# Optimization experiments

Hardware: AMD Instinct MI355X
Metric: run time of the kernel (lower is better)

The kernel has to match this reference:

```python
import jax, jax.numpy as jnp
import numpy as np

B, C, H, W = 4, 512, 96, 96
NH = 8
HD = C // NH
NC = 128
D = 768
L = H * W
EPS = 1e-5  # torch LayerNorm default


def _l2n(x, axis):
    # F.normalize: x / max(||x||, 1e-12)
    return x / jnp.maximum(jnp.linalg.norm(x, axis=axis, keepdims=True), 1e-12)


def _ln2d(x, g, b):
    # LayerNorm2d: normalize over channel dim of (B,C,H,W)
    mu = x.mean(1, keepdims=True)
    var = ((x - mu) ** 2).mean(1, keepdims=True)
    return (x - mu) / jnp.sqrt(var + EPS) * g[None, :, None, None] + b[None, :, None, None]


def _conv1x1(x, w):
    return jnp.einsum('oc,bchw->bohw', w, x)


def setup_inputs() -> dict:
    key = jax.random.key(0)
    ks = jax.random.split(key, 9)
    s = 0.02
    return {
        'img_feats': jax.random.normal(ks[0], (B, C, H, W), jnp.float32),
        'cls_embs': jax.random.normal(ks[1], (NC, D), jnp.float32),
        'cls_logits': jax.random.normal(ks[2], (B, NC), jnp.float32),
        'seg_logits': jax.random.normal(ks[3], (B, 1, H, W), jnp.float32),
        'gamma_g': jnp.ones((D,), jnp.float32), 'beta_g': jnp.zeros((D,), jnp.float32),
        'gamma_f': jnp.ones((C,), jnp.float32), 'beta_f': jnp.zeros((C,), jnp.float32),
        'attn_scale': jnp.ones((NH, 1, 1), jnp.float32),
        'Wg': jax.random.normal(ks[4], (C, D), jnp.float32) * s,
        'Wqkv': jax.random.normal(ks[5], (3 * C, C), jnp.float32) * s,
        'Wo': jax.random.normal(ks[6], (C, C), jnp.float32) * s,
        'bo': jnp.zeros((C,), jnp.float32),
        'gamma_n': jnp.ones((C,), jnp.float32), 'beta_n': jnp.zeros((C,), jnp.float32),
        'W1': jax.random.normal(ks[7], (C, C), jnp.float32) * s, 'b1': jnp.zeros((C,), jnp.float32),
        'W2': jax.random.normal(ks[8], (C, C), jnp.float32) * s, 'b2': jnp.zeros((C,), jnp.float32),
    }


def reference(img_feats, cls_embs, cls_logits, seg_logits, gamma_g, beta_g,
              gamma_f, beta_f, attn_scale, Wg, Wqkv, Wo, bo, gamma_n, beta_n,
              W1, b1, W2, b2):
    xn = _ln2d(img_feats, gamma_f, beta_f)
    # guide LayerNorm over embedding dim
    mu = cls_embs.mean(-1, keepdims=True)
    var = ((cls_embs - mu) ** 2).mean(-1, keepdims=True)
    cn = (cls_embs - mu) / jnp.sqrt(var + EPS) * gamma_g + beta_g
    g = (cn @ Wg.T).reshape(NC, NH, HD)  # nc nh hd

    qkv = _conv1x1(xn, Wqkv).reshape(B, 3, NH, HD, L)
    q, k, v = qkv[:, 0], qkv[:, 1], qkv[:, 2]  # each (B,NH,HD,L)

    # cosine guide map + min-max normalization + softmax-weighted aggregation over classes
    gm = jnp.einsum('nhd,bhdl->bhnl', _l2n(g, -1), _l2n(q, -2))
    gm = gm - gm.min(-1, keepdims=True)
    gm = gm / gm.max(-1, keepdims=True)
    gm = (jax.nn.softmax(gm, axis=2) * gm).sum(2, keepdims=True)  # (B,NH,1,L)

    # auxiliary guide map from cls logits + masked pooling of k
    cls_obj = jnp.einsum('nhd,bn->bhd', g, cls_logits)
    mask = jax.nn.sigmoid(seg_logits)  # (B,1,H,W)
    seg_obj = (mask * k.reshape(B, C, H, W)).sum((2, 3)) / mask.sum((2, 3))  # (B,C)
    obj = _l2n(cls_obj + seg_obj.reshape(B, NH, HD), -1)
    aux = jnp.einsum('bhd,bhdl->bhl', obj, _l2n(k, -2))[:, :, None, :]
    aux = aux - aux.min(-1, keepdims=True)
    aux = aux / aux.max(-1, keepdims=True)
    gm = gm * aux

    v = gm * v
    # channel (transposed) cosine attention: (B,NH,HD,HD)
    attn = jnp.einsum('bhdl,bhel->bhde', _l2n(q, -1), _l2n(k, -1)) * attn_scale
    out = jnp.einsum('bhde,bhel->bhdl', jax.nn.softmax(attn, -1), v).reshape(B, C, H, W)

    x = img_feats + _conv1x1(out, Wo) + bo[None, :, None, None]
    # ConvMlp with pre-norm: LayerNorm2d -> 1x1 conv -> GELU -> 1x1 conv
    fin = _ln2d(x, gamma_n, beta_n)
    h = jax.nn.gelu(_conv1x1(fin, W1) + b1[None, :, None, None], approximate=False)
    return x + _conv1x1(h, W2) + b2[None, :, None, None]
```

## Files before the change

kernel.cpp:

```cpp
#include <hip/hip_runtime.h>
#include <hip/hip_bf16.h>
#include <math.h>

#define BB 4
#define CC 512
#define NHEAD 8
#define HDIM 64
#define NCLS 128
#define DD 768
#define LL 9216
#define BLPIX 36864
#define EPSV 1e-5f
#define GMBLK 144
#define AUXBLK 36
#define LSPLIT 8

typedef __hip_bfloat16 bf16;
typedef __attribute__((ext_vector_type(8))) short short8v;
typedef __attribute__((ext_vector_type(4))) short short4v;
typedef __attribute__((ext_vector_type(4))) float f32x4;

__device__ __forceinline__ float bf2f(bf16 v){ return __bfloat162float(v); }
__device__ __forceinline__ bf16 f2bf(float v){ return __float2bfloat16(v); }
__device__ __forceinline__ short bfbits(float v){ bf16 b = __float2bfloat16(v); return *reinterpret_cast<short*>(&b); }
__device__ __forceinline__ float s2f(short s){ bf16 b = *reinterpret_cast<bf16*>(&s); return __bfloat162float(b); }

__global__ void ln_stats_k(const float* __restrict__ X, float* __restrict__ mu, float* __restrict__ rs){
  int idx = blockIdx.x * blockDim.x + threadIdx.x;
  if (idx >= BLPIX) return;
  int b = idx / LL, l = idx % LL;
  const float* p = X + (size_t)b * CC * LL + l;
  float s = 0.f, ss = 0.f;
  #pragma unroll 8
  for (int c = 0; c < CC; c++){ float v = p[(size_t)c * LL]; s += v; ss += v * v; }
  float m = s * (1.0f / CC);
  float var = ss * (1.0f / CC) - m * m;
  mu[idx] = m; rs[idx] = rsqrtf(var + EPSV);
}

__global__ __launch_bounds__(256) void lnT_k(const float* __restrict__ X,
    const float* __restrict__ mu, const float* __restrict__ rs,
    const float* __restrict__ lng, const float* __restrict__ lnb,
    bf16* __restrict__ out){
  __shared__ float t[64][65];
  int c0 = blockIdx.x * 64;
  int p0 = blockIdx.y * 64;
  int b = p0 / LL;
  int l0 = p0 - b * LL;
  int tid = threadIdx.x;
  #pragma unroll
  for (int i = 0; i < 16; i++){
    int idx = i * 256 + tid;
    int cl = idx >> 6, ll2 = idx & 63;
    t[cl][ll2] = X[(size_t)b * CC * LL + (size_t)(c0 + cl) * LL + l0 + ll2];
  }
  __syncthreads();
  int pr = tid >> 4;
  int cc = (tid & 15) * 4;
  #pragma unroll
  for (int i = 0; i < 4; i++){
    int pl = pr + i * 16;
    int p = p0 + pl;
    float m = mu[p], r = rs[p];
    short4v pk;
    #pragma unroll
    for (int e = 0; e < 4; e++){
      int c = c0 + cc + e;
      float v = (t[cc + e][pl] - m) * r * lng[c] + lnb[c];
      pk[e] = bfbits(v);
    }
    *(short4v*)&out[(size_t)p * CC + c0 + cc] = pk;
  }
}

__global__ void wcast_k(const float* __restrict__ wqkv, const float* __restrict__ wo,
                        const float* __restrict__ w1, const float* __restrict__ w2,
                        bf16* __restrict__ oq, bf16* __restrict__ oo,
                        bf16* __restrict__ o1, bf16* __restrict__ o2){
  int i = blockIdx.x * 256 + threadIdx.x;
  int e = i * 4;
  const float* src; bf16* dst; int off;
  if (e < 786432){ src = wqkv; dst = oq; off = e; }
  else if (e < 1048576){ src = wo; dst = oo; off = e - 786432; }
  else if (e < 1310720){ src = w1; dst = o1; off = e - 1048576; }
  else { src = w2; dst = o2; off = e - 1310720; }
  float4 v = *reinterpret_cast<const float4*>(src + off);
  short4v pk;
  pk[0] = bfbits(v.x); pk[1] = bfbits(v.y); pk[2] = bfbits(v.z); pk[3] = bfbits(v.w);
  *(short4v*)&dst[off] = pk;
}

__global__ void statsred_k(const float2* __restrict__ statp, float* __restrict__ mu, float* __restrict__ rs){
  int p = blockIdx.x * 256 + threadIdx.x;
  if (p >= BLPIX) return;
  float s = 0.f, ss = 0.f;
  #pragma unroll
  for (int part = 0; part < 4; part++){
    float2 v = statp[part * BLPIX + p];
    s += v.x; ss += v.y;
  }
  float m = s * (1.0f / CC);
  float var = ss * (1.0f / CC) - m * m;
  mu[p] = m; rs[p] = rsqrtf(var + EPSV);
}

template<int MODE>
__global__ __launch_bounds__(256, 2) void mgemm_k(
    const bf16* __restrict__ A,
    const bf16* __restrict__ B,
    const float* __restrict__ residf,
    const bf16*  __restrict__ residb,
    const float* __restrict__ bias,
    const float* __restrict__ mu, const float* __restrict__ rs,
    const float* __restrict__ lng, const float* __restrict__ lnb,
    float2* __restrict__ statp,
    bf16* __restrict__ qo, bf16* __restrict__ ko, bf16* __restrict__ vo,
    bf16* __restrict__ xT_out,
    float* __restrict__ xo,
    bf16* __restrict__ ho)
{
  __shared__ short Asm[128 * 64];
  __shared__ short Bsm[128 * 64];
  __shared__ float sred[4][4][16][2];
  int tid = threadIdx.x;
  int lane = tid & 63, wv = tid >> 6;
  int wr = wv >> 1, wc = wv & 1;
  int r15 = lane & 15, g = lane >> 4, h7 = lane & 7;
  int gx = gridDim.x;
  int flat = blockIdx.y * gx + blockIdx.x;
  int cpx = (gx * gridDim.y) >> 3;
  int swz = (flat & 7) * cpx + (flat >> 3);
  int m0 = (swz % gx) * 128, n0 = (swz / gx) * 128;
  int srow = tid >> 3, skkg = tid & 7;
  int sslot = ((skkg ^ (srow & 7))) * 8;

  f32x4 acc[4][4];
  #pragma unroll
  for (int i = 0; i < 4; i++)
    #pragma unroll
    for (int j = 0; j < 4; j++) acc[i][j] = (f32x4){0.f, 0.f, 0.f, 0.f};

  short8v pa[4], pb[4];
  auto loadAB = [&](int it){
    int k0 = it * 64;
    if (MODE == 2){
      int c0 = k0 + skkg * 8;
      float ga[8], be[8];
      *(float4*)&ga[0] = *(const float4*)&lng[c0];
      *(float4*)&ga[4] = *(const float4*)&lng[c0 + 4];
      *(float4*)&be[0] = *(const float4*)&lnb[c0];
      *(float4*)&be[4] = *(const float4*)&lnb[c0 + 4];
      #pragma unroll
      for (int r = 0; r < 4; r++){
        pa[r] = *reinterpret_cast<const short8v*>(A + (size_t)(m0 + r * 32 + srow) * 512 + c0);
        int rp = n0 + r * 32 + srow;
        float mm = mu[rp], rr = rs[rp];
        short8v raw = *reinterpret_cast<const short8v*>(B + (size_t)rp * 512 + c0);
        short8v ov;
        #pragma unroll
        for (int e = 0; e < 8; e++){
          float v = (s2f(raw[e]) - mm) * rr * ga[e] + be[e];
          ov[e] = bfbits(v);
        }
        pb[r] = ov;
      }
    } else {
      #pragma unroll
      for (int r = 0; r < 4; r++){
        pa[r] = *reinterpret_cast<const short8v*>(A + (size_t)(m0 + r * 32 + srow) * 512 + k0 + skkg * 8);
        pb[r] = *reinterpret_cast<const short8v*>(B + (size_t)(n0 + r * 32 + srow) * 512 + k0 + skkg * 8);
      }
    }
  };

  loadAB(0);
  for (int it = 0; it < 8; ++it){
    __syncthreads();
    #pragma unroll
    for (int r = 0; r < 4; r++){
      int row = r * 32 + srow;
      *(short8v*)&Asm[row * 64 + sslot] = pa[r];
      *(short8v*)&Bsm[row * 64 + sslot] = pb[r];
    }
    __syncthreads();
    if (it < 7) loadAB(it + 1);
    #pragma unroll
    for (int s = 0; s < 2; s++){
      int slot = ((s * 4 + g) ^ h7) * 8;
      short8v af[4], bf_[4];
      #pragma unroll
      for (int i = 0; i < 4; i++){
        af[i]  = *(const short8v*)&Asm[(wr * 64 + i * 16 + r15) * 64 + slot];
        bf_[i] = *(const short8v*)&Bsm[(wc * 64 + i * 16 + r15) * 64 + slot];
      }
      #pragma unroll
      for (int i = 0; i < 4; i++)
        #pragma unroll
        for (int j = 0; j < 4; j++){
          if (MODE == 2)
            acc[i][j] = __builtin_amdgcn_mfma_f32_16x16x32_bf16(bf_[i], af[j], acc[i][j], 0, 0, 0);
          else
            acc[i][j] = __builtin_amdgcn_mfma_f32_16x16x32_bf16(af[i], bf_[j], acc[i][j], 0, 0, 0);
        }
    }
  }

  int bIdx = n0 / LL;
  int lbase = n0 - bIdx * LL;
  if (MODE == 0){
    int part = m0 >> 9;
    if (part < 2){
      bf16* dst = (part == 0) ? qo : ko;
      int chb = (m0 & 511) + wr * 64;
      #pragma unroll
      for (int i = 0; i < 4; i++)
        #pragma unroll
        for (int j = 0; j < 4; j++){
          int l = lbase + wc * 64 + j * 16 + r15;
          #pragma unroll
          for (int e = 0; e < 4; e++){
            int ch = chb + i * 16 + g * 4 + e;
            dst[(size_t)bIdx * CC * LL + (size_t)ch * LL + l] = f2bf(acc[i][j][e]);
          }
        }
    } else {
      int chb = (m0 & 511) + wr * 64;
      #pragma unroll
      for (int i = 0; i < 4; i++)
        #pragma unroll
        for (int j = 0; j < 4; j++){
          int l = lbase + wc * 64 + j * 16 + r15;
          int ch = chb + i * 16 + g * 4;
          short4v pk;
          #pragma unroll
          for (int e = 0; e < 4; e++) pk[e] = bfbits(acc[i][j][e]);
          *(short4v*)&vo[((size_t)bIdx * LL + l) * CC + ch] = pk;
        }
    }
  } else if (MODE == 1){
    float sj[4] = {0.f,0.f,0.f,0.f}, ssj[4] = {0.f,0.f,0.f,0.f};
    #pragma unroll
    for (int i = 0; i < 4; i++)
      #pragma unroll
      for (int j = 0; j < 4; j++){
        int l = lbase + wc * 64 + j * 16 + r15;
        int chm = m0 + wr * 64 + i * 16 + g * 4;
        short4v pk;
        #pragma unroll
        for (int e = 0; e < 4; e++){
          int m = chm + e;
          size_t o = (size_t)bIdx * CC * LL + (size_t)m * LL + l;
          float xv = residf[o] + acc[i][j][e] + bias[m];
          pk[e] = bfbits(xv);
          sj[j] += xv; ssj[j] += xv * xv;
        }
        *(short4v*)&xT_out[((size_t)bIdx * LL + l) * CC + chm] = pk;
      }
    #pragma unroll
    for (int j = 0; j < 4; j++){
      sj[j] += __shfl_xor(sj[j], 16); sj[j] += __shfl_xor(sj[j], 32);
      ssj[j] += __shfl_xor(ssj[j], 16); ssj[j] += __shfl_xor(ssj[j], 32);
    }
    if (g == 0){
      #pragma unroll
      for (int j = 0; j < 4; j++){ sred[wv][j][r15][0] = sj[j]; sred[wv][j][r15][1] = ssj[j]; }
    }
    __syncthreads();
    if (tid < 128){
      int wv2 = tid >> 6, lane2 = tid & 63, j2 = lane2 >> 4, r2 = lane2 & 15;
      float s = sred[wv2][j2][r2][0] + sred[wv2 + 2][j2][r2][0];
      float ss2 = sred[wv2][j2][r2][1] + sred[wv2 + 2][j2][r2][1];
      int p = n0 + wv2 * 64 + j2 * 16 + r2;
      statp[(m0 >> 7) * BLPIX + p] = make_float2(s, ss2);
    }
  } else if (MODE == 3){
    #pragma unroll
    for (int i = 0; i < 4; i++)
      #pragma unroll
      for (int j = 0; j < 4; j++){
        int l = lbase + wc * 64 + j * 16 + r15;
        int chm = m0 + wr * 64 + i * 16 + g * 4;
        short4v rv = *(const short4v*)&residb[((size_t)bIdx * LL + l) * CC + chm];
        #pragma unroll
        for (int e = 0; e < 4; e++){
          int m = chm + e;
          size_t o = (size_t)bIdx * CC * LL + (size_t)m * LL + l;
          xo[o] = s2f(rv[e]) + acc[i][j][e] + bias[m];
        }
      }
  } else {
    #pragma unroll
    for (int i = 0; i < 4; i++)
      #pragma unroll
      for (int j = 0; j < 4; j++){
        int mm = m0 + wr * 64 + j * 16 + r15;
        float bv = bias[mm];
        #pragma unroll
        for (int e = 0; e < 4; e++){
          int n = n0 + wc * 64 + i * 16 + g * 4 + e;
          float t = acc[i][j][e] + bv;
          float gv = 0.5f * t * (1.0f + erff(t * 0.70710678118654752f));
          ho[(size_t)n * CC + mm] = f2bf(gv);
        }
      }
  }
}

__global__ void rownorm_k(const bf16* __restrict__ q, const bf16* __restrict__ k,
                          float* __restrict__ qn, float* __restrict__ kn){
  __shared__ float red[256];
  int row = blockIdx.x;
  const bf16* src = (row < 2048) ? q : k;
  int r = (row < 2048) ? row : row - 2048;
  const bf16* p = src + (size_t)r * LL;
  float s = 0.f;
  for (int i = threadIdx.x; i < LL; i += 256){ float v = bf2f(p[i]); s += v * v; }
  red[threadIdx.x] = s; __syncthreads();
  for (int st = 128; st > 0; st >>= 1){ if (threadIdx.x < st) red[threadIdx.x] += red[threadIdx.x + st]; __syncthreads(); }
  if (threadIdx.x == 0){
    float nv = fmaxf(sqrtf(red[0]), 1e-12f);
    if (row < 2048) qn[r] = nv; else kn[r] = nv;
  }
}

__global__ void clsg_k(const float* __restrict__ cls_embs, const float* __restrict__ gamma_g,
                       const float* __restrict__ beta_g, const float* __restrict__ Wg,
                       float* __restrict__ g, bf16* __restrict__ gnb){
  __shared__ float cn[DD];
  __shared__ float red[256];
  __shared__ float gsh[CC];
  __shared__ float nrm[NHEAD];
  int n = blockIdx.x;
  const float* e = cls_embs + (size_t)n * DD;
  float s = 0.f, ss = 0.f;
  for (int i = threadIdx.x; i < DD; i += 256){ float v = e[i]; s += v; ss += v * v; }
  red[threadIdx.x] = s; __syncthreads();
  for (int st = 128; st > 0; st >>= 1){ if (threadIdx.x < st) red[threadIdx.x] += red[threadIdx.x + st]; __syncthreads(); }
  float mean = red[0] / DD; __syncthreads();
  red[threadIdx.x] = ss; __syncthreads();
  for (int st = 128; st > 0; st >>= 1){ if (threadIdx.x < st) red[threadIdx.x] += red[threadIdx.x + st]; __syncthreads(); }
  float var = red[0] / DD - mean * mean;
  float rstd = rsqrtf(var + EPSV);
  __syncthreads();
  for (int i = threadIdx.x; i < DD; i += 256) cn[i] = (e[i] - mean) * rstd * gamma_g[i] + beta_g[i];
  __syncthreads();
  for (int c = threadIdx.x; c < CC; c += 256){
    const float* w = Wg + (size_t)c * DD;
    float a = 0.f;
    #pragma unroll 8
    for (int d = 0; d < DD; d++) a += cn[d] * w[d];
    gsh[c] = a;
  }
  __syncthreads();
  if (threadIdx.x < NHEAD){
    float a = 0.f;
    for (int d = 0; d < HDIM; d++){ float v = gsh[threadIdx.x * HDIM + d]; a += v * v; }
    nrm[threadIdx.x] = fmaxf(sqrtf(a), 1e-12f);
  }
  __syncthreads();
  for (int c = threadIdx.x; c < CC; c += 256){
    g[(size_t)n * CC + c] = gsh[c];
    gnb[(size_t)n * CC + c] = f2bf(gsh[c] / nrm[c >> 6]);
  }
}

__global__ void clsobj_k(const float* __restrict__ g, const float* __restrict__ cls_l,
                         float* __restrict__ cls_obj){
  int idx = blockIdx.x * 256 + threadIdx.x;
  if (idx >= BB * CC) return;
  int b = idx >> 9, c = idx & 511;
  float a = 0.f;
  for (int n = 0; n < NCLS; n++) a += g[(size_t)n * CC + c] * cls_l[b * NCLS + n];
  cls_obj[idx] = a;
}

__global__ __launch_bounds__(256) void gm1_k(const bf16* __restrict__ q, const bf16* __restrict__ gnb,
        float* __restrict__ pmin, float* __restrict__ pmax){
  __shared__ bf16 qs[64 * 68];
  __shared__ float sspart[4][64];
  __shared__ float rq[64];
  int bh = blockIdx.x, lt = blockIdx.y;
  int l0 = lt * 64;
  int t = threadIdx.x;
  int b = bh >> 3, h = bh & 7;
  int w = t >> 6, lane = t & 63, r15 = lane & 15, g = lane >> 4;
  const bf16* qp = q + (size_t)b * CC * LL + (size_t)h * HDIM * LL + l0;
  #pragma unroll
  for (int i2 = 0; i2 < 4; i2++){
    int idx = t + i2 * 256;
    int d = idx >> 4, lch = (idx & 15) * 4;
    short4v vv = *reinterpret_cast<const short4v*>(qp + (size_t)d * LL + lch);
    *(short4v*)&qs[d * 68 + lch] = vv;
  }
  __syncthreads();
  {
    int l = t & 63, dg = t >> 6;
    float ss = 0.f;
    #pragma unroll
    for (int dd = 0; dd < 16; dd++){ float v = bf2f(qs[(dg * 16 + dd) * 68 + l]); ss += v * v; }
    sspart[dg][l] = ss;
  }
  __syncthreads();
  if (t < 64){
    float ss = sspart[0][t] + sspart[1][t] + sspart[2][t] + sspart[3][t];
    rq[t] = 1.0f / fmaxf(sqrtf(ss), 1e-12f);
  }
  __syncthreads();
  short8v ag[2][2];
  #pragma unroll
  for (int i = 0; i < 2; i++)
    #pragma unroll
    for (int kt = 0; kt < 2; kt++)
      ag[i][kt] = *reinterpret_cast<const short8v*>(gnb + (size_t)(w * 32 + i * 16 + r15) * CC + h * 64 + kt * 32 + g * 8);
  short8v bq[4][2];
  #pragma unroll
  for (int j = 0; j < 4; j++){
    float rqv = rq[j * 16 + r15];
    #pragma unroll
    for (int kt = 0; kt < 2; kt++){
      short8v bb;
      #pragma unroll
      for (int jj = 0; jj < 8; jj++){
        int d = kt * 32 + g * 8 + jj;
        bb[jj] = bfbits(bf2f(qs[d * 68 + j * 16 + r15]) * rqv);
      }
      bq[j][kt] = bb;
    }
  }
  f32x4 acc[2][4];
  #pragma unroll
  for (int i = 0; i < 2; i++)
    #pragma unroll
    for (int j = 0; j < 4; j++) acc[i][j] = (f32x4){0.f,0.f,0.f,0.f};
  #pragma unroll
  for (int kt = 0; kt < 2; kt++)
    #pragma unroll
    for (int i = 0; i < 2; i++)
      #pragma unroll
      for (int j = 0; j < 4; j++)
        acc[i][j] = __builtin_amdgcn_mfma_f32_16x16x32_bf16(ag[i][kt], bq[j][kt], acc[i][j], 0, 0, 0);
  #pragma unroll
  for (int i = 0; i < 2; i++)
    #pragma unroll
    for (int e = 0; e < 4; e++){
      float mn = acc[i][0][e], mx = acc[i][0][e];
      #pragma unroll
      for (int j = 1; j < 4; j++){ mn = fminf(mn, acc[i][j][e]); mx = fmaxf(mx, acc[i][j][e]); }
      #pragma unroll
      for (int msk = 1; msk < 16; msk <<= 1){
        mn = fminf(mn, __shfl_xor(mn, msk));
        mx = fmaxf(mx, __shfl_xor(mx, msk));
      }
      if (r15 == 0){
        int n = w * 32 + i * 16 + g * 4 + e;
        pmin[((size_t)bh * 128 + n) * GMBLK + lt] = mn;
        pmax[((size_t)bh * 128 + n) * GMBLK + lt] = mx;
      }
    }
}

__global__ void gmred_k(const float* __restrict__ pmin, const float* __restrict__ pmax,
                        float* __restrict__ gmin, float* __restrict__ gms){
  __shared__ float rmn[64], rmx[64];
  int row = blockIdx.x;
  float mn = 1e30f, mx = -1e30f;
  for (int i = threadIdx.x; i < GMBLK; i += 64){
    mn = fminf(mn, pmin[(size_t)row * GMBLK + i]);
    mx = fmaxf(mx, pmax[(size_t)row * GMBLK + i]);
  }
  rmn[threadIdx.x] = mn; rmx[threadIdx.x] = mx; __syncthreads();
  for (int st = 32; st > 0; st >>= 1){
    if (threadIdx.x < st){
      rmn[threadIdx.x] = fminf(rmn[threadIdx.x], rmn[threadIdx.x + st]);
      rmx[threadIdx.x] = fmaxf(rmx[threadIdx.x], rmx[threadIdx.x + st]);
    }
    __syncthreads();
  }
  if (threadIdx.x == 0){ gmin[row] = rmn[0]; gms[row] = rmx[0] - rmn[0]; }
}

__global__ void seg_k(const float* __restrict__ seg, const bf16* __restrict__ k, float* __restrict__ seg_num){
  __shared__ float red[256];
  int bc = blockIdx.x;
  int b = bc >> 9;
  const bf16* p = k + (size_t)bc * LL;
  const float* sp = seg + (size_t)b * LL;
  float s = 0.f;
  for (int i = threadIdx.x; i < LL; i += 256){
    float m = 1.0f / (1.0f + expf(-sp[i]));
    s += m * bf2f(p[i]);
  }
  red[threadIdx.x] = s; __syncthreads();
  for (int st = 128; st > 0; st >>= 1){ if (threadIdx.x < st) red[threadIdx.x] += red[threadIdx.x + st]; __syncthreads(); }
  if (threadIdx.x == 0) seg_num[bc] = red[0];
}

__global__ void segden_k(const float* __restrict__ seg, float* __restrict__ den){
  __shared__ float red[256];
  int b = blockIdx.x;
  const float* sp = seg + (size_t)b * LL;
  float s = 0.f;
  for (int i = threadIdx.x; i < LL; i += 256) s += 1.0f / (1.0f + expf(-sp[i]));
  red[threadIdx.x] = s; __syncthreads();
  for (int st = 128; st > 0; st >>= 1){ if (threadIdx.x < st) red[threadIdx.x] += red[threadIdx.x + st]; __syncthreads(); }
  if (threadIdx.x == 0) den[b] = red[0];
}

__global__ void obj_k(const float* __restrict__ cls_obj, const float* __restrict__ seg_num,
                      const float* __restrict__ den, float* __restrict__ obj){
  __shared__ float sval[2048];
  __shared__ float nrm[32];
  int tid = threadIdx.x;
  #pragma unroll
  for (int i = 0; i < 8; i++){
    int idx = tid + i * 256;
    int b = idx >> 9;
    sval[idx] = cls_obj[idx] + seg_num[idx] / den[b];
  }
  __syncthreads();
  if (tid < 32){
    float s = 0.f;
    for (int d = 0; d < 64; d++){ float v = sval[tid * 64 + d]; s += v * v; }
    nrm[tid] = fmaxf(sqrtf(s), 1e-12f);
  }
  __syncthreads();
  #pragma unroll
  for (int i = 0; i < 8; i++){
    int idx = tid + i * 256;
    obj[idx] = sval[idx] / nrm[idx >> 6];
  }
}

__global__ void aux_k(const bf16* __restrict__ k, const float* __restrict__ obj, float* __restrict__ aux,
                      float* __restrict__ pmin, float* __restrict__ pmax){
  __shared__ float os[64];
  __shared__ float rmn[256], rmx[256];
  int bh = blockIdx.x, lt = blockIdx.y;
  int b = bh >> 3, h = bh & 7;
  int l = lt * 256 + threadIdx.x;
  if (threadIdx.x < 64) os[threadIdx.x] = obj[bh * 64 + threadIdx.x];
  __syncthreads();
  const bf16* kp = k + (size_t)b * CC * LL + (size_t)h * HDIM * LL + l;
  float ss = 0.f, dot = 0.f;
  #pragma unroll 8
  for (int d = 0; d < 64; d++){ float v = bf2f(kp[(size_t)d * LL]); ss += v * v; dot += os[d] * v; }
  float av = dot / fmaxf(sqrtf(ss), 1e-12f);
  aux[(size_t)bh * LL + l] = av;
  rmn[threadIdx.x] = av; rmx[threadIdx.x] = av; __syncthreads();
  for (int st = 128; st > 0; st >>= 1){
    if (threadIdx.x < st){
      rmn[threadIdx.x] = fminf(rmn[threadIdx.x], rmn[threadIdx.x + st]);
      rmx[threadIdx.x] = fmaxf(rmx[threadIdx.x], rmx[threadIdx.x + st]);
    }
    __syncthreads();
  }
  if (threadIdx.x == 0){ pmin[bh * AUXBLK + lt] = rmn[0]; pmax[bh * AUXBLK + lt] = rmx[0]; }
}

__global__ void auxred_k(const float* __restrict__ pmin, const float* __restrict__ pmax,
                         float* __restrict__ amin, float* __restrict__ ams){
  __shared__ float rmn[64], rmx[64];
  int bh = blockIdx.x;
  float mn = 1e30f, mx = -1e30f;
  for (int i = threadIdx.x; i < AUXBLK; i += 64){
    mn = fminf(mn, pmin[bh * AUXBLK + i]);
    mx = fmaxf(mx, pmax[bh * AUXBLK + i]);
  }
  rmn[threadIdx.x] = mn; rmx[threadIdx.x] = mx; __syncthreads();
  for (int st = 32; st > 0; st >>= 1){
    if (threadIdx.x < st){
      rmn[threadIdx.x] = fminf(rmn[threadIdx.x], rmn[threadIdx.x + st]);
      rmx[threadIdx.x] = fmaxf(rmx[threadIdx.x], rmx[threadIdx.x + st]);
    }
    __syncthreads();
  }
  if (threadIdx.x == 0){ amin[bh] = rmn[0]; ams[bh] = rmx[0] - rmn[0]; }
}

__global__ __launch_bounds__(256) void attn_k(const bf16* __restrict__ q, const bf16* __restrict__ k,
                                              float* __restrict__ part){
  __shared__ float red[4 * 4096];
  int ls = blockIdx.x, bh = blockIdx.y;
  int b = bh >> 3, h = bh & 7;
  int t = threadIdx.x;
  int w = t >> 6, lane = t & 63, r15 = lane & 15, g = lane >> 4;
  const bf16* qp = q + (size_t)b * CC * LL + (size_t)h * HDIM * LL;
  const bf16* kp = k + (size_t)b * CC * LL + (size_t)h * HDIM * LL;
  int kbase = ls * 1152 + w * 288;
  f32x4 acc[4][4];
  #pragma unroll
  for (int i = 0; i < 4; i++)
    #pragma unroll
    for (int j = 0; j < 4; j++) acc[i][j] = (f32x4){0.f,0.f,0.f,0.f};
  for (int ks = 0; ks < 9; ks++){
    int koff = kbase + ks * 32 + g * 8;
    short8v aq[4], bk[4];
    #pragma unroll
    for (int i = 0; i < 4; i++) aq[i] = *reinterpret_cast<const short8v*>(qp + (size_t)(i * 16 + r15) * LL + koff);
    #pragma unroll
    for (int j = 0; j < 4; j++) bk[j] = *reinterpret_cast<const short8v*>(kp + (size_t)(j * 16 + r15) * LL + koff);
    #pragma unroll
    for (int i = 0; i < 4; i++)
      #pragma unroll
      for (int j = 0; j < 4; j++)
        acc[i][j] = __builtin_amdgcn_mfma_f32_16x16x32_bf16(aq[i], bk[j], acc[i][j], 0, 0, 0);
  }
  #pragma unroll
  for (int i = 0; i < 4; i++)
    #pragma unroll
    for (int j = 0; j < 4; j++)
      #pragma unroll
      for (int e = 0; e < 4; e++)
        red[w * 4096 + (i * 16 + g * 4 + e) * 64 + j * 16 + r15] = acc[i][j][e];
  __syncthreads();
  #pragma unroll
  for (int it = 0; it < 16; it++){
    int idx = t + it * 256;
    part[((size_t)(bh * LSPLIT + ls)) * 4096 + idx] = red[idx] + red[4096 + idx] + red[8192 + idx] + red[12288 + idx];
  }
}

__global__ void smax_k(const float* __restrict__ part, const float* __restrict__ qn,
                       const float* __restrict__ kn, const float* __restrict__ scale,
                       bf16* __restrict__ Pb){
  __shared__ float As[64 * 65];
  int bh = blockIdx.x;
  int h = bh & 7;
  int tid = threadIdx.x;
  #pragma unroll
  for (int i = 0; i < 16; i++){
    int cell = tid + i * 256;
    int d = cell >> 6, e = cell & 63;
    float s = 0.f;
    #pragma unroll
    for (int ls = 0; ls < LSPLIT; ls++) s += part[((size_t)(bh * LSPLIT + ls)) * 4096 + cell];
    As[d * 65 + e] = s * scale[h] / (qn[bh * 64 + d] * kn[bh * 64 + e]);
  }
  __syncthreads();
  if (tid < 64){
    int d = tid;
    float mx = -1e30f;
    for (int e = 0; e < 64; e++) mx = fmaxf(mx, As[d * 65 + e]);
    float sum = 0.f;
    for (int e = 0; e < 64; e++){ float ev = expf(As[d * 65 + e] - mx); As[d * 65 + e] = ev; sum += ev; }
    float inv = 1.0f / sum;
    for (int e = 0; e < 64; e++) Pb[(size_t)bh * 4096 + d * 64 + e] = f2bf(As[d * 65 + e] * inv);
  }
}

__global__ __launch_bounds__(256) void pv_k(const bf16* __restrict__ q, const bf16* __restrict__ gnb,
      const float* __restrict__ aux,
      const float* __restrict__ gmin, const float* __restrict__ gms,
      const float* __restrict__ amin, const float* __restrict__ ams,
      const bf16* __restrict__ Pb, const bf16* __restrict__ vT, bf16* __restrict__ outT){
  __shared__ bf16 qs[64 * 68];
  __shared__ float sspart[4][64];
  __shared__ float rq[64];
  __shared__ float gminS[128], rgmsS[128];
  __shared__ float separt[4][64], setpart[4][64];
  __shared__ float wl[64];
  int bh = blockIdx.x, lt = blockIdx.y;
  int l0 = lt * 64;
  int t = threadIdx.x;
  int b = bh >> 3, h = bh & 7;
  int w = t >> 6, lane = t & 63, r15 = lane & 15, g = lane >> 4;
  if (t < 128){ gminS[t] = gmin[bh * 128 + t]; rgmsS[t] = 1.0f / gms[bh * 128 + t]; }
  const bf16* qp = q + (size_t)b * CC * LL + (size_t)h * HDIM * LL + l0;
  #pragma unroll
  for (int i2 = 0; i2 < 4; i2++){
    int idx = t + i2 * 256;
    int d = idx >> 4, lch = (idx & 15) * 4;
    short4v vv = *reinterpret_cast<const short4v*>(qp + (size_t)d * LL + lch);
    *(short4v*)&qs[d * 68 + lch] = vv;
  }
  __syncthreads();
  {
    int l = t & 63, dg = t >> 6;
    float ss = 0.f;
    #pragma unroll
    for (int dd = 0; dd < 16; dd++){ float v = bf2f(qs[(dg * 16 + dd) * 68 + l]); ss += v * v; }
    sspart[dg][l] = ss;
  }
  __syncthreads();
  if (t < 64){
    float ss = sspart[0][t] + sspart[1][t] + sspart[2][t] + sspart[3][t];
    rq[t] = 1.0f / fmaxf(sqrtf(ss), 1e-12f);
  }
  __syncthreads();
  short8v ag[2][2];
  #pragma unroll
  for (int i = 0; i < 2; i++)
    #pragma unroll
    for (int kt = 0; kt < 2; kt++)
      ag[i][kt] = *reinterpret_cast<const short8v*>(gnb + (size_t)(w * 32 + i * 16 + r15) * CC + h * 64 + kt * 32 + g * 8);
  short8v bq[4][2];
  #pragma unroll
  for (int j = 0; j < 4; j++){
    float rqv = rq[j * 16 + r15];
    #pragma unroll
    for (int kt = 0; kt < 2; kt++){
      short8v bb;
      #pragma unroll
      for (int jj = 0; jj < 8; jj++){
        int d = kt * 32 + g * 8 + jj;
        bb[jj] = bfbits(bf2f(qs[d * 68 + j * 16 + r15]) * rqv);
      }
      bq[j][kt] = bb;
    }
  }
  f32x4 acc[2][4];
  #pragma unroll
  for (int i = 0; i < 2; i++)
    #pragma unroll
    for (int j = 0; j < 4; j++) acc[i][j] = (f32x4){0.f,0.f,0.f,0.f};
  #pragma unroll
  for (int kt = 0; kt < 2; kt++)
    #pragma unroll
    for (int i = 0; i < 2; i++)
      #pragma unroll
      for (int j = 0; j < 4; j++)
        acc[i][j] = __builtin_amdgcn_mfma_f32_16x16x32_bf16(ag[i][kt], bq[j][kt], acc[i][j], 0, 0, 0);
  float seL[4] = {0.f,0.f,0.f,0.f}, setL[4] = {0.f,0.f,0.f,0.f};
  #pragma unroll
  for (int i = 0; i < 2; i++)
    #pragma unroll
    for (int j = 0; j < 4; j++)
      #pragma unroll
      for (int e = 0; e < 4; e++){
        int n = w * 32 + i * 16 + g * 4 + e;
        float tt = (acc[i][j][e] - gminS[n]) * rgmsS[n];
        float ee = __expf(tt);
        seL[j] += ee; setL[j] += ee * tt;
      }
  #pragma unroll
  for (int j = 0; j < 4; j++){
    seL[j] += __shfl_xor(seL[j], 16); seL[j] += __shfl_xor(seL[j], 32);
    setL[j] += __shfl_xor(setL[j], 16); setL[j] += __shfl_xor(setL[j], 32);
  }
  if (g == 0){
    #pragma unroll
    for (int j = 0; j < 4; j++){ separt[w][j * 16 + r15] = seL[j]; setpart[w][j * 16 + r15] = setL[j]; }
  }
  __syncthreads();
  if (t < 64){
    float se = separt[0][t] + separt[1][t] + separt[2][t] + separt[3][t];
    float st = setpart[0][t] + setpart[1][t] + setpart[2][t] + setpart[3][t];
    float gmred = st / se;
    float auxn = (aux[(size_t)bh * LL + l0 + t] - amin[bh]) / ams[bh];
    wl[t] = gmred * auxn;
  }
  __syncthreads();
  short8v ap[4][2];
  #pragma unroll
  for (int i = 0; i < 4; i++)
    #pragma unroll
    for (int kt = 0; kt < 2; kt++)
      ap[i][kt] = *reinterpret_cast<const short8v*>(Pb + (size_t)bh * 4096 + (i * 16 + r15) * 64 + kt * 32 + g * 8);
  const bf16* vrow = vT + ((size_t)b * LL + l0 + w * 16 + r15) * CC + h * 64;
  short8v bv[2];
  #pragma unroll
  for (int kt = 0; kt < 2; kt++) bv[kt] = *reinterpret_cast<const short8v*>(vrow + kt * 32 + g * 8);
  f32x4 oacc[4];
  #pragma unroll
  for (int i = 0; i < 4; i++) oacc[i] = (f32x4){0.f,0.f,0.f,0.f};
  #pragma unroll
  for (int kt = 0; kt < 2; kt++)
    #pragma unroll
    for (int i = 0; i < 4; i++)
      oacc[i] = __builtin_amdgcn_mfma_f32_16x16x32_bf16(ap[i][kt], bv[kt], oacc[i], 0, 0, 0);
  float wlv = wl[w * 16 + r15];
  bf16* orow = outT + ((size_t)b * LL + l0 + w * 16 + r15) * CC + h * 64;
  #pragma unroll
  for (int i = 0; i < 4; i++){
    short4v pk;
    #pragma unroll
    for (int e = 0; e < 4; e++) pk[e] = bfbits(oacc[i][e] * wlv);
    *(short4v*)&orow[i * 16 + g * 4] = pk;
  }
}

extern "C" void kernel_launch(void* const* d_in, const int* in_sizes, int n_in,
                              void* d_out, int out_size, void* d_ws, size_t ws_size,
                              hipStream_t stream){
  const float* img        = (const float*)d_in[0];
  const float* cls_embs   = (const float*)d_in[1];
  const float* cls_logits = (const float*)d_in[2];
  const float* seg        = (const float*)d_in[3];
  const float* gamma_g    = (const float*)d_in[4];
  const float* beta_g     = (const float*)d_in[5];
  const float* gamma_f    = (const float*)d_in[6];
  const float* beta_f     = (const float*)d_in[7];
  const float* attn_scale = (const float*)d_in[8];
  const float* Wg         = (const float*)d_in[9];
  const float* Wqkv       = (const float*)d_in[10];
  const float* Wo         = (const float*)d_in[11];
  const float* bo         = (const float*)d_in[12];
  const float* gamma_n    = (const float*)d_in[13];
  const float* beta_n     = (const float*)d_in[14];
  const float* W1         = (const float*)d_in[15];
  const float* b1         = (const float*)d_in[16];
  const float* W2         = (const float*)d_in[17];
  const float* b2         = (const float*)d_in[18];
  float* outp = (float*)d_out;
  (void)in_sizes; (void)n_in; (void)out_size;

  char* wsb = (char*)d_ws;
  size_t off = 0;
  auto alloc = [&](size_t bytes)->char*{
    char* p = wsb + off;
    off += (bytes + 255) & ~(size_t)255;
    return p;
  };
  float* mu1   = (float*)alloc((size_t)BLPIX * 4);
  float* rs1   = (float*)alloc((size_t)BLPIX * 4);
  float2* statp= (float2*)alloc((size_t)4 * BLPIX * 8);
  float* qn    = (float*)alloc(2048 * 4);
  float* kn    = (float*)alloc(2048 * 4);
  float* gbuf  = (float*)alloc((size_t)NCLS * CC * 4);
  bf16*  gnbb  = (bf16*)alloc((size_t)NCLS * CC * 2);
  float* clsov = (float*)alloc(2048 * 4);
  float* segn  = (float*)alloc(2048 * 4);
  float* segd  = (float*)alloc(256);
  float* objv  = (float*)alloc(2048 * 4);
  float* gminp = (float*)alloc((size_t)32 * 128 * GMBLK * 4);
  float* gmaxp = (float*)alloc((size_t)32 * 128 * GMBLK * 4);
  float* gminv = (float*)alloc(4096 * 4);
  float* gmsv  = (float*)alloc(4096 * 4);
  float* auxv  = (float*)alloc((size_t)32 * LL * 4);
  float* apmin = (float*)alloc(32 * AUXBLK * 4);
  float* apmax = (float*)alloc(32 * AUXBLK * 4);
  float* aminv = (float*)alloc(256);
  float* amsv  = (float*)alloc(256);
  bf16*  Pb    = (bf16*)alloc((size_t)32 * 4096 * 2);
  float* apart = (float*)alloc((size_t)32 * LSPLIT * 4096 * 4);
  bf16* qb    = (bf16*)alloc((size_t)BB * CC * LL * 2);
  bf16* kb    = (bf16*)alloc((size_t)BB * CC * LL * 2);
  bf16* wqkvb = (bf16*)alloc((size_t)1536 * 512 * 2);
  bf16* wob   = (bf16*)alloc((size_t)512 * 512 * 2);
  bf16* w1b   = (bf16*)alloc((size_t)512 * 512 * 2);
  bf16* w2b   = (bf16*)alloc((size_t)512 * 512 * 2);
  bf16* vT  = (bf16*)d_out;
  bf16* xnT = (bf16*)((char*)d_out + (size_t)BB * CC * LL * 2);
  bf16* outT = kb;
  bf16* xT   = qb;
  bf16* hbT  = kb;
  if (off > ws_size) return;

  ln_stats_k<<<BLPIX / 256, 256, 0, stream>>>(img, mu1, rs1);
  wcast_k<<<1536, 256, 0, stream>>>(Wqkv, Wo, W1, W2, wqkvb, wob, w1b, w2b);
  lnT_k<<<dim3(8, 576), 256, 0, stream>>>(img, mu1, rs1, gamma_f, beta_f, xnT);
  mgemm_k<0><<<dim3(12, 288), 256, 0, stream>>>(wqkvb, xnT, nullptr, nullptr, nullptr,
      nullptr, nullptr, nullptr, nullptr, nullptr, qb, kb, vT, nullptr, nullptr, nullptr);
  rownorm_k<<<4096, 256, 0, stream>>>(qb, kb, qn, kn);
  clsg_k<<<NCLS, 256, 0, stream>>>(cls_embs, gamma_g, beta_g, Wg, gbuf, gnbb);
  clsobj_k<<<8, 256, 0, stream>>>(gbuf, cls_logits, clsov);
  gm1_k<<<dim3(32, GMBLK), 256, 0, stream>>>(qb, gnbb, gminp, gmaxp);
  gmred_k<<<4096, 64, 0, stream>>>(gminp, gmaxp, gminv, gmsv);
  seg_k<<<2048, 256, 0, stream>>>(seg, kb, segn);
  segden_k<<<BB, 256, 0, stream>>>(seg, segd);
  obj_k<<<1, 256, 0, stream>>>(clsov, segn, segd, objv);
  aux_k<<<dim3(32, AUXBLK), 256, 0, stream>>>(kb, objv, auxv, apmin, apmax);
  auxred_k<<<32, 64, 0, stream>>>(apmin, apmax, aminv, amsv);
  attn_k<<<dim3(LSPLIT, 32), 256, 0, stream>>>(qb, kb, apart);
  smax_k<<<32, 256, 0, stream>>>(apart, qn, kn, attn_scale, Pb);
  pv_k<<<dim3(32, GMBLK), 256, 0, stream>>>(qb, gnbb, auxv, gminv, gmsv, aminv, amsv, Pb, vT, outT);
  mgemm_k<1><<<dim3(4, 288), 256, 0, stream>>>(wob, outT, img, nullptr, bo,
      nullptr, nullptr, nullptr, nullptr, statp, nullptr, nullptr, nullptr, xT, nullptr, nullptr);
  statsred_k<<<BLPIX / 256, 256, 0, stream>>>(statp, mu1, rs1);
  mgemm_k<2><<<dim3(4, 288), 256, 0, stream>>>(w1b, xT, nullptr, nullptr, b1,
      mu1, rs1, gamma_n, beta_n, nullptr, nullptr, nullptr, nullptr, nullptr, nullptr, hbT);
  mgemm_k<3><<<dim3(4, 288), 256, 0, stream>>>(w2b, hbT, nullptr, xT, b2,
      nullptr, nullptr, nullptr, nullptr, nullptr, nullptr, nullptr, nullptr, nullptr, outp, nullptr);
}
```

Measured before the change: 497.6 us.

## Fuse LayerNorm stats into transpose and q/k row norms into QKV GEMM epilogue

Merges the per-pixel LayerNorm statistics kernel with the normalize-and-transpose kernel, so each block computes stats for 64 pixels and then writes all 512 channels. The QKV GEMM epilogue now emits per-tile sum-of-squares partials for the q and k rows. A small reduction kernel replaces the full rownorm pass, which reread all of q and k. The fused LN kernel launches only 576 blocks, each looping serially over channels, which lowers parallelism, and the GEMM epilogue gains shuffles and a barrier.

```diff
diff --git a/kernel.cpp b/kernel.cpp
--- a/kernel.cpp
+++ b/kernel.cpp
@@ -14,6 +14,7 @@
 #define GMBLK 144
 #define AUXBLK 36
 #define LSPLIT 8
+#define NLT 72
 
 typedef __hip_bfloat16 bf16;
 typedef __attribute__((ext_vector_type(8))) short short8v;
@@ -25,51 +26,57 @@
 __device__ __forceinline__ short bfbits(float v){ bf16 b = __float2bfloat16(v); return *reinterpret_cast<short*>(&b); }
 __device__ __forceinline__ float s2f(short s){ bf16 b = *reinterpret_cast<bf16*>(&s); return __bfloat162float(b); }
 
-__global__ void ln_stats_k(const float* __restrict__ X, float* __restrict__ mu, float* __restrict__ rs){
-  int idx = blockIdx.x * blockDim.x + threadIdx.x;
-  if (idx >= BLPIX) return;
-  int b = idx / LL, l = idx % LL;
-  const float* p = X + (size_t)b * CC * LL + l;
+__global__ __launch_bounds__(256) void fuse_ln_k(const float* __restrict__ X,
+    const float* __restrict__ lng, const float* __restrict__ lnb,
+    bf16* __restrict__ xnT){
+  __shared__ float sred[2][4][64];
+  __shared__ float muS[64], rsS[64];
+  __shared__ float t[64][65];
+  int p0 = blockIdx.x * 64;
+  int b = p0 / LL, l0 = p0 - b * LL;
+  int tid = threadIdx.x;
+  int cg = tid >> 6, l = tid & 63;
+  const float* base = X + (size_t)b * CC * LL + l0 + l;
   float s = 0.f, ss = 0.f;
-  #pragma unroll 8
-  for (int c = 0; c < CC; c++){ float v = p[(size_t)c * LL]; s += v; ss += v * v; }
-  float m = s * (1.0f / CC);
-  float var = ss * (1.0f / CC) - m * m;
-  mu[idx] = m; rs[idx] = rsqrtf(var + EPSV);
-}
-
-__global__ __launch_bounds__(256) void lnT_k(const float* __restrict__ X,
-    const float* __restrict__ mu, const float* __restrict__ rs,
-    const float* __restrict__ lng, const float* __restrict__ lnb,
-    bf16* __restrict__ out){
-  __shared__ float t[64][65];
-  int c0 = blockIdx.x * 64;
-  int p0 = blockIdx.y * 64;
-  int b = p0 / LL;
-  int l0 = p0 - b * LL;
-  int tid = threadIdx.x;
-  #pragma unroll
-  for (int i = 0; i < 16; i++){
-    int idx = i * 256 + tid;
-    int cl = idx >> 6, ll2 = idx & 63;
-    t[cl][ll2] = X[(size_t)b * CC * LL + (size_t)(c0 + cl) * LL + l0 + ll2];
+  for (int c = cg * 128; c < cg * 128 + 128; c++){
+    float v = base[(size_t)c * LL];
+    s += v; ss += v * v;
+  }
+  sred[0][cg][l] = s; sred[1][cg][l] = ss;
+  __syncthreads();
+  if (tid < 64){
+    float st = sred[0][0][tid] + sred[0][1][tid] + sred[0][2][tid] + sred[0][3][tid];
+    float sst = sred[1][0][tid] + sred[1][1][tid] + sred[1][2][tid] + sred[1][3][tid];
+    float m = st * (1.0f / CC);
+    float var = sst * (1.0f / CC) - m * m;
+    muS[tid] = m; rsS[tid] = rsqrtf(var + EPSV);
   }
   __syncthreads();
   int pr = tid >> 4;
   int cc = (tid & 15) * 4;
-  #pragma unroll
-  for (int i = 0; i < 4; i++){
-    int pl = pr + i * 16;
-    int p = p0 + pl;
-    float m = mu[p], r = rs[p];
-    short4v pk;
-    #pragma unroll
-    for (int e = 0; e < 4; e++){
-      int c = c0 + cc + e;
-      float v = (t[cc + e][pl] - m) * r * lng[c] + lnb[c];
-      pk[e] = bfbits(v);
-    }
-    *(short4v*)&out[(size_t)p * CC + c0 + cc] = pk;
+  for (int cb = 0; cb < 8; cb++){
+    int c0 = cb * 64;
+    #pragma unroll
+    for (int i = 0; i < 16; i++){
+      int idx = i * 256 + tid;
+      int cl = idx >> 6, ll2 = idx & 63;
+      t[cl][ll2] = X[(size_t)b * CC * LL + (size_t)(c0 + cl) * LL + l0 + ll2];
+    }
+    __syncthreads();
+    #pragma unroll
+    for (int i = 0; i < 4; i++){
+      int pl = pr + i * 16;
+      int p = p0 + pl;
+      float m = muS[pl], r = rsS[pl];
+      short4v pk;
+      #pragma unroll
+      for (int e = 0; e < 4; e++){
+        int c = c0 + cc + e;
+        pk[e] = bfbits((t[cc + e][pl] - m) * r * lng[c] + lnb[c]);
+      }
+      *(short4v*)&xnT[(size_t)p * CC + c0 + cc] = pk;
+    }
+    __syncthreads();
   }
 }
 
@@ -104,16 +111,32 @@
   mu[p] = m; rs[p] = rsqrtf(var + EPSV);
 }
 
+__global__ void rownorm_red_k(const float* __restrict__ qssp, const float* __restrict__ kssp,
+                              float* __restrict__ qn, float* __restrict__ kn){
+  int row = blockIdx.x;
+  const float* src = (row < 2048) ? qssp : kssp;
+  int r = (row < 2048) ? row : row - 2048;
+  float s = 0.f;
+  for (int i = threadIdx.x; i < NLT; i += 64) s += src[(size_t)r * NLT + i];
+  #pragma unroll
+  for (int m = 1; m < 64; m <<= 1) s += __shfl_xor(s, m);
+  if (threadIdx.x == 0){
+    float nv = fmaxf(sqrtf(s), 1e-12f);
+    if (row < 2048) qn[r] = nv; else kn[r] = nv;
+  }
+}
+
 template<int MODE>
 __global__ __launch_bounds__(256, 2) void mgemm_k(
     const bf16* __restrict__ A,
     const bf16* __restrict__ B,
     const float* __restrict__ residf,
-    const bf16*  __restrict__ residb,
+    const bf16* __restrict__ residb,
     const float* __restrict__ bias,
     const float* __restrict__ mu, const float* __restrict__ rs,
     const float* __restrict__ lng, const float* __restrict__ lnb,
     float2* __restrict__ statp,
+    float* __restrict__ qssp, float* __restrict__ kssp,
     bf16* __restrict__ qo, bf16* __restrict__ ko, bf16* __restrict__ vo,
     bf16* __restrict__ xT_out,
     float* __restrict__ xo,
@@ -121,7 +144,7 @@
 {
   __shared__ short Asm[128 * 64];
   __shared__ short Bsm[128 * 64];
-  __shared__ float sred[4][4][16][2];
+  __shared__ float sredf[512];
   int tid = threadIdx.x;
   int lane = tid & 63, wv = tid >> 6;
   int wr = wv >> 1, wc = wv & 1;
@@ -223,6 +246,26 @@
             dst[(size_t)bIdx * CC * LL + (size_t)ch * LL + l] = f2bf(acc[i][j][e]);
           }
         }
+      #pragma unroll
+      for (int i = 0; i < 4; i++)
+        #pragma unroll
+        for (int e = 0; e < 4; e++){
+          float ssv = acc[i][0][e]*acc[i][0][e] + acc[i][1][e]*acc[i][1][e]
+                    + acc[i][2][e]*acc[i][2][e] + acc[i][3][e]*acc[i][3][e];
+          #pragma unroll
+          for (int msk = 1; msk < 16; msk <<= 1) ssv += __shfl_xor(ssv, msk);
+          if (r15 == 0) sredf[wv * 64 + i * 16 + g * 4 + e] = ssv;
+        }
+      __syncthreads();
+      if (tid < 128){
+        int wrr = tid >> 6, chL = tid & 63;
+        float tot = sredf[(wrr * 2) * 64 + chL] + sredf[(wrr * 2 + 1) * 64 + chL];
+        int c = (m0 & 511) + wrr * 64 + chL;
+        int row = bIdx * 512 + c;
+        int ltile = lbase >> 7;
+        float* dd = (part == 0) ? qssp : kssp;
+        dd[(size_t)row * NLT + ltile] = tot;
+      }
     } else {
       int chb = (m0 & 511) + wr * 64;
       #pragma unroll
@@ -263,13 +306,16 @@
     }
     if (g == 0){
       #pragma unroll
-      for (int j = 0; j < 4; j++){ sred[wv][j][r15][0] = sj[j]; sred[wv][j][r15][1] = ssj[j]; }
+      for (int j = 0; j < 4; j++){
+        sredf[wv * 128 + j * 32 + r15 * 2 + 0] = sj[j];
+        sredf[wv * 128 + j * 32 + r15 * 2 + 1] = ssj[j];
+      }
     }
     __syncthreads();
     if (tid < 128){
       int wv2 = tid >> 6, lane2 = tid & 63, j2 = lane2 >> 4, r2 = lane2 & 15;
-      float s = sred[wv2][j2][r2][0] + sred[wv2 + 2][j2][r2][0];
-      float ss2 = sred[wv2][j2][r2][1] + sred[wv2 + 2][j2][r2][1];
+      float s   = sredf[wv2 * 128 + j2 * 32 + r2 * 2 + 0] + sredf[(wv2 + 2) * 128 + j2 * 32 + r2 * 2 + 0];
+      float ss2 = sredf[wv2 * 128 + j2 * 32 + r2 * 2 + 1] + sredf[(wv2 + 2) * 128 + j2 * 32 + r2 * 2 + 1];
       int p = n0 + wv2 * 64 + j2 * 16 + r2;
       statp[(m0 >> 7) * BLPIX + p] = make_float2(s, ss2);
     }
@@ -303,23 +349,6 @@
           ho[(size_t)n * CC + mm] = f2bf(gv);
         }
       }
-  }
-}
-
-__global__ void rownorm_k(const bf16* __restrict__ q, const bf16* __restrict__ k,
-                          float* __restrict__ qn, float* __restrict__ kn){
-  __shared__ float red[256];
-  int row = blockIdx.x;
-  const bf16* src = (row < 2048) ? q : k;
-  int r = (row < 2048) ? row : row - 2048;
-  const bf16* p = src + (size_t)r * LL;
-  float s = 0.f;
-  for (int i = threadIdx.x; i < LL; i += 256){ float v = bf2f(p[i]); s += v * v; }
-  red[threadIdx.x] = s; __syncthreads();
-  for (int st = 128; st > 0; st >>= 1){ if (threadIdx.x < st) red[threadIdx.x] += red[threadIdx.x + st]; __syncthreads(); }
-  if (threadIdx.x == 0){
-    float nv = fmaxf(sqrtf(red[0]), 1e-12f);
-    if (row < 2048) qn[r] = nv; else kn[r] = nv;
   }
 }
 
@@ -814,6 +843,8 @@
   float* mu1   = (float*)alloc((size_t)BLPIX * 4);
   float* rs1   = (float*)alloc((size_t)BLPIX * 4);
   float2* statp= (float2*)alloc((size_t)4 * BLPIX * 8);
+  float* qssp  = (float*)alloc((size_t)2048 * NLT * 4);
+  float* kssp  = (float*)alloc((size_t)2048 * NLT * 4);
   float* qn    = (float*)alloc(2048 * 4);
   float* kn    = (float*)alloc(2048 * 4);
   float* gbuf  = (float*)alloc((size_t)NCLS * CC * 4);
@@ -846,12 +877,12 @@
   bf16* hbT  = kb;
   if (off > ws_size) return;
 
-  ln_stats_k<<<BLPIX / 256, 256, 0, stream>>>(img, mu1, rs1);
   wcast_k<<<1536, 256, 0, stream>>>(Wqkv, Wo, W1, W2, wqkvb, wob, w1b, w2b);
-  lnT_k<<<dim3(8, 576), 256, 0, stream>>>(img, mu1, rs1, gamma_f, beta_f, xnT);
+  fuse_ln_k<<<576, 256, 0, stream>>>(img, gamma_f, beta_f, xnT);
   mgemm_k<0><<<dim3(12, 288), 256, 0, stream>>>(wqkvb, xnT, nullptr, nullptr, nullptr,
-      nullptr, nullptr, nullptr, nullptr, nullptr, qb, kb, vT, nullptr, nullptr, nullptr);
-  rownorm_k<<<4096, 256, 0, stream>>>(qb, kb, qn, kn);
+      nullptr, nullptr, nullptr, nullptr, nullptr, qssp, kssp,
+      qb, kb, vT, nullptr, nullptr, nullptr);
+  rownorm_red_k<<<4096, 64, 0, stream>>>(qssp, kssp, qn, kn);
   clsg_k<<<NCLS, 256, 0, stream>>>(cls_embs, gamma_g, beta_g, Wg, gbuf, gnbb);
   clsobj_k<<<8, 256, 0, stream>>>(gbuf, cls_logits, clsov);
   gm1_k<<<dim3(32, GMBLK), 256, 0, stream>>>(qb, gnbb, gminp, gmaxp);
@@ -865,10 +896,13 @@
   smax_k<<<32, 256, 0, stream>>>(apart, qn, kn, attn_scale, Pb);
   pv_k<<<dim3(32, GMBLK), 256, 0, stream>>>(qb, gnbb, auxv, gminv, gmsv, aminv, amsv, Pb, vT, outT);
   mgemm_k<1><<<dim3(4, 288), 256, 0, stream>>>(wob, outT, img, nullptr, bo,
-      nullptr, nullptr, nullptr, nullptr, statp, nullptr, nullptr, nullptr, xT, nullptr, nullptr);
+      nullptr, nullptr, nullptr, nullptr, statp, nullptr, nullptr,
+      nullptr, nullptr, nullptr, xT, nullptr, nullptr);
   statsred_k<<<BLPIX / 256, 256, 0, stream>>>(statp, mu1, rs1);
   mgemm_k<2><<<dim3(4, 288), 256, 0, stream>>>(w1b, xT, nullptr, nullptr, b1,
-      mu1, rs1, gamma_n, beta_n, nullptr, nullptr, nullptr, nullptr, nullptr, nullptr, hbT);
+      mu1, rs1, gamma_n, beta_n, nullptr, nullptr, nullptr,
+      nullptr, nullptr, nullptr, nullptr, nullptr, hbT);
   mgemm_k<3><<<dim3(4, 288), 256, 0, stream>>>(w2b, hbT, nullptr, xT, b2,
-      nullptr, nullptr, nullptr, nullptr, nullptr, nullptr, nullptr, nullptr, nullptr, outp, nullptr);
-}
+      nullptr, nullptr, nullptr, nullptr, nullptr, nullptr, nullptr,
+      nullptr, nullptr, nullptr, nullptr, outp, nullptr);
+}
```

New measurement: 463.8 us. -6.8%, faster.
